# Kernel tuning notes

Hardware: AMD Instinct MI355X
Metric: run time of the kernel (lower is better)

The kernel has to match this reference:

```python
import jax, jax.numpy as jnp
import numpy as np

# Grid constants from init_kwargs: output_shape = [1, 10, 200, 176, 64]
D, H, W, C = 10, 200, 176, 64
N_VOX = 30000


def _conv_block(x, w, scale, bias, stride, pad):
    # x: [N,C,D,H,W]; w: [O,I,kd,kh,kw]; ZeroPad3d then valid Conv3d,
    # then fused (inference) BatchNorm3d + ReLU.
    x = jnp.pad(x, ((0, 0), (0, 0), (pad[0], pad[0]), (pad[1], pad[1]), (pad[2], pad[2])))
    x = jax.lax.conv_general_dilated(
        x, w, window_strides=stride, padding='VALID',
        dimension_numbers=('NCDHW', 'OIDHW', 'NCDHW'))
    s = scale[None, :, None, None, None]
    b = bias[None, :, None, None, None]
    return jax.nn.relu(x * s + b)


def setup_inputs() -> dict:
    key = jax.random.key(0)
    kf, kd, kh, kw, k1, k2, k3, ks = jax.random.split(key, 8)
    voxel_features = jax.random.normal(kf, (N_VOX, C), dtype=jnp.float32)
    # coors columns: (batch_idx, d, h, w) each in range
    b_idx = jnp.zeros((N_VOX,), dtype=jnp.int32)  # batch_size = 1
    d_idx = jax.random.randint(kd, (N_VOX,), 0, D, dtype=jnp.int32)
    h_idx = jax.random.randint(kh, (N_VOX,), 0, H, dtype=jnp.int32)
    w_idx = jax.random.randint(kw, (N_VOX,), 0, W, dtype=jnp.int32)
    coors = jnp.stack([b_idx, d_idx, h_idx, w_idx], axis=1)
    fan = 1.0 / np.sqrt(C * 27)
    W1 = jax.random.normal(k1, (64, C, 3, 3, 3), dtype=jnp.float32) * fan
    W2 = jax.random.normal(k2, (64, 64, 3, 3, 3), dtype=jnp.float32) * fan
    W3 = jax.random.normal(k3, (64, 64, 3, 3, 3), dtype=jnp.float32) * fan
    ks1, ks2, ks3 = jax.random.split(ks, 3)
    scale1 = jax.random.uniform(ks1, (64,), dtype=jnp.float32, minval=0.5, maxval=1.5)
    scale2 = jax.random.uniform(ks2, (64,), dtype=jnp.float32, minval=0.5, maxval=1.5)
    scale3 = jax.random.uniform(ks3, (64,), dtype=jnp.float32, minval=0.5, maxval=1.5)
    bias1 = jax.random.normal(jax.random.fold_in(ks1, 1), (64,), dtype=jnp.float32) * 0.1
    bias2 = jax.random.normal(jax.random.fold_in(ks2, 1), (64,), dtype=jnp.float32) * 0.1
    bias3 = jax.random.normal(jax.random.fold_in(ks3, 1), (64,), dtype=jnp.float32) * 0.1
    return {
        'voxel_features': voxel_features, 'coors': coors, 'batch_size': 1,
        'W1': W1, 'scale1': scale1, 'bias1': bias1,
        'W2': W2, 'scale2': scale2, 'bias2': bias2,
        'W3': W3, 'scale3': scale3, 'bias3': bias3,
    }


def reference(voxel_features, coors, batch_size,
              W1, scale1, bias1, W2, scale2, bias2, W3, scale3, bias3):
    # scatter_nd: sparse voxel features -> dense [B, D, H, W, C]
    dense = jnp.zeros((batch_size, D, H, W, C), dtype=voxel_features.dtype)
    dense = dense.at[coors[:, 0], coors[:, 1], coors[:, 2], coors[:, 3]].set(voxel_features)
    x = dense.transpose(0, 4, 1, 2, 3)  # [B, C, D, H, W]
    # middle_conv: Pad(1)+Conv3d s=(2,1,1); Pad(0,1,1)+Conv3d s=1; Pad(1)+Conv3d s=(2,1,1)
    x = _conv_block(x, W1, scale1, bias1, (2, 1, 1), (1, 1, 1))   # D: 10 -> 5
    x = _conv_block(x, W2, scale2, bias2, (1, 1, 1), (0, 1, 1))   # D: 5 -> 3
    x = _conv_block(x, W3, scale3, bias3, (2, 1, 1), (1, 1, 1))   # D: 3 -> 2
    N, Cc, Dd, Hh, Ww = x.shape
    return x.reshape(N, Cc * Dd, Hh, Ww)  # [B, 128, H, W]
```

## Files before the change

kernel.cpp:

```cpp
#include <hip/hip_runtime.h>
#include <cstddef>

#define HH 200
#define WW 176
#define HP 202
#define WP 178
#define D_IN 10
#define D1 5
#define D2 3
#define D3 2
#define SLICE ((size_t)HP * WP * 64)

#define LA_BYTES 38912

typedef _Float16 h8 __attribute__((ext_vector_type(8)));
typedef float f4 __attribute__((ext_vector_type(4)));

__device__ __forceinline__ void gl_lds16(const void* g, void* l) {
    __builtin_amdgcn_global_load_lds(
        (const __attribute__((address_space(1))) void*)g,
        (__attribute__((address_space(3))) void*)l, 16, 0, 0);
}

__global__ __launch_bounds__(256) void prep_k(const float* __restrict__ W1,
                                              const float* __restrict__ W2,
                                              const float* __restrict__ W3,
                                              _Float16* __restrict__ wdst,
                                              _Float16* __restrict__ A2,
                                              _Float16* __restrict__ A3,
                                              const int* __restrict__ coors,
                                              int* __restrict__ winner, int nvox) {
    const int b = blockIdx.x;
    if (b < 8) {
        _Float16* base = (b < D1) ? (A2 + (size_t)b * SLICE) : (A3 + (size_t)(b - D1) * SLICE);
        const h8 z = {};
        for (int t = threadIdx.x; t < 6080; t += 256) {
            size_t off;
            if (t < 2848) {
                int r = t / 1424, c = t - r * 1424;
                off = (size_t)(r ? (HP - 1) : 0) * WP * 64 + (size_t)c * 8;
            } else {
                int u = t - 2848;
                int c = u / 1616, v = u - c * 1616;
                int hr = v >> 3, o = v & 7;
                off = ((size_t)hr * WP + (c ? (WP - 1) : 0)) * 64 + (size_t)o * 8;
            }
            *(h8*)(base + off) = z;
        }
    } else if (b < 8 + 1296) {
        int idx = (b - 8) * 256 + threadIdx.x;
        if (idx < 3 * 27 * 64 * 64) {
            int set = idx / 110592;
            int r = idx - set * 110592;
            const float* src = set == 0 ? W1 : (set == 1 ? W2 : W3);
            int ci = r & 63;
            int co = (r >> 6) & 63;
            int tap = r >> 12;
            wdst[set * 110592 + tap * 4096 + (ci >> 3) * 512 + co * 8 + (ci & 7)] =
                (_Float16)src[(co * 64 + ci) * 27 + tap];
        }
    } else {
        int v = (b - 1304) * 256 + threadIdx.x;
        if (v < nvox) {
            int d = coors[v * 4 + 1], h = coors[v * 4 + 2], w = coors[v * 4 + 3];
            atomicMax(&winner[(d * HH + h) * WW + w], v + 1);
        }
    }
}

__global__ __launch_bounds__(256) void scatter_k(const float* __restrict__ feat,
                                                 const int* __restrict__ coors,
                                                 const int* __restrict__ winner,
                                                 _Float16* __restrict__ A, int nvox) {
    int v = blockIdx.x * 4 + (threadIdx.x >> 6);
    int ci = threadIdx.x & 63;
    if (v >= nvox) return;
    int d = coors[v * 4 + 1], h = coors[v * 4 + 2], w = coors[v * 4 + 3];
    if (winner[(d * HH + h) * WW + w] != v + 1) return;
    int P = w + 1;
    int swz = (((ci >> 3) ^ (P & 7)) << 3) | (ci & 7);
    A[(size_t)d * SLICE + ((size_t)(h + 1) * WP + P) * 64 + swz] = (_Float16)feat[v * 64 + ci];
}

template <int FINAL>
__global__ __launch_bounds__(256, 4) void conv_mfma_k(
    const _Float16* __restrict__ in, void* __restrict__ outp,
    const _Float16* __restrict__ wt,
    const float* __restrict__ scale, const float* __restrict__ bias,
    int inD, int strideD, int padD) {
    __shared__ char smem_raw[LA_BYTES];
    _Float16* la = (_Float16*)smem_raw;

    const int lane = threadIdx.x & 63;
    const int wave = threadIdx.x >> 6;
    const int l16 = lane & 15;
    const int quad = lane >> 4;
    const int h0 = blockIdx.y * 4;
    const int wb = blockIdx.x * 48;
    const int d = blockIdx.z;

    int kd_lo = padD - d * strideD; if (kd_lo < 0) kd_lo = 0;
    int kd_hi = inD - 1 - d * strideD + padD; if (kd_hi > 2) kd_hi = 2;

    f4 acc[3][4];
#pragma unroll
    for (int mt = 0; mt < 3; ++mt)
#pragma unroll
        for (int nt = 0; nt < 4; ++nt) acc[mt][nt] = (f4){0.f, 0.f, 0.f, 0.f};

    for (int kd = kd_lo; kd <= kd_hi; ++kd) {
        const int zd = d * strideD + kd - padD;
        const _Float16* __restrict__ aplane = in + (size_t)zd * SLICE;
        const _Float16* __restrict__ wkd = wt + (size_t)kd * 9 * 4096;

        __syncthreads();
        for (int j = wave; j < 38; j += 4) {
            int c = j * 64 + lane;
            if (c > 2399) c = 2399;
            int r = c / 400;
            int rem = c - r * 400;
            int px = rem >> 3, s = rem & 7;
            int g = wb + px; if (g > 177) g = 177;
            gl_lds16(aplane + ((size_t)(h0 + r) * WP + g) * 64 + s * 8,
                     smem_raw + j * 1024);
        }
        __syncthreads();

#pragma unroll
        for (int t = 0; t < 9; ++t) {
            const int kh = t / 3;
            const int kw = t - 3 * kh;

            h8 b[2][4];
#pragma unroll
            for (int ch = 0; ch < 2; ++ch)
#pragma unroll
                for (int nt = 0; nt < 4; ++nt)
                    b[ch][nt] = *(const h8*)(wkd + t * 4096 +
                                             ((ch * 4 + quad) << 9) +
                                             ((nt * 16 + l16) << 3));

#pragma unroll
            for (int ch = 0; ch < 2; ++ch) {
                const int q = ch * 4 + quad;
#pragma unroll
                for (int mt = 0; mt < 3; ++mt) {
                    const int px = mt * 16 + l16 + kw;
                    h8 a = *(const h8*)(la + ((wave + kh) * 50 + px) * 64 +
                                        ((q ^ (px & 7)) << 3));
#pragma unroll
                    for (int nt = 0; nt < 4; ++nt)
                        acc[mt][nt] = __builtin_amdgcn_mfma_f32_16x16x32_f16(
                            a, b[ch][nt], acc[mt][nt], 0, 0, 0);
                }
            }
        }
    }

    const int h = h0 + wave;
#pragma unroll
    for (int nt = 0; nt < 4; ++nt) {
        const int co = nt * 16 + l16;
        const float s = scale[co];
        const float bb = bias[co];
#pragma unroll
        for (int mt = 0; mt < 3; ++mt) {
            const int w0 = wb + mt * 16 + quad * 4;
            if (w0 < WW) {
                if (FINAL) {
                    f4 v;
#pragma unroll
                    for (int r = 0; r < 4; ++r) {
                        float x = acc[mt][nt][r] * s + bb;
                        v[r] = x > 0.f ? x : 0.f;
                    }
                    *(f4*)((float*)outp + (((size_t)(co * 2 + d)) * HH + h) * WW + w0) = v;
                } else {
#pragma unroll
                    for (int r = 0; r < 4; ++r) {
                        float x = acc[mt][nt][r] * s + bb;
                        x = x > 0.f ? x : 0.f;
                        const int P = w0 + r + 1;
                        const int swz = (((co >> 3) ^ (P & 7)) << 3) | (co & 7);
                        ((_Float16*)outp)[(size_t)d * SLICE +
                            ((size_t)(h + 1) * WP + P) * 64 + swz] = (_Float16)x;
                    }
                }
            }
        }
    }
}

extern "C" void kernel_launch(void* const* d_in, const int* in_sizes, int n_in,
                              void* d_out, int out_size, void* d_ws, size_t ws_size,
                              hipStream_t stream) {
    const float* feat   = (const float*)d_in[0];
    const int*   coors  = (const int*)d_in[1];
    const float* W1     = (const float*)d_in[3];
    const float* scale1 = (const float*)d_in[4];
    const float* bias1  = (const float*)d_in[5];
    const float* W2     = (const float*)d_in[6];
    const float* scale2 = (const float*)d_in[7];
    const float* bias2  = (const float*)d_in[8];
    const float* W3     = (const float*)d_in[9];
    const float* scale3 = (const float*)d_in[10];
    const float* bias3  = (const float*)d_in[11];
    const int nvox = in_sizes[0] / 64;

    const size_t nA1 = (size_t)D_IN * SLICE;
    const size_t nWin = (size_t)D_IN * HH * WW;
    const size_t nA2 = (size_t)D1 * SLICE;
    const size_t nA3 = (size_t)D2 * SLICE;
    const size_t nWT = (size_t)27 * 64 * 64;

    _Float16* A1 = (_Float16*)d_ws;
    int* win = (int*)(A1 + nA1);
    _Float16* A2 = (_Float16*)(win + nWin);
    _Float16* A3 = A2 + nA2;
    _Float16* wt1 = A3 + nA3;
    _Float16* wt2 = wt1 + nWT;
    _Float16* wt3 = wt2 + nWT;

    hipMemsetAsync(d_ws, 0, nA1 * sizeof(_Float16) + nWin * sizeof(int), stream);

    const int win_blk = (nvox + 255) / 256;
    prep_k<<<8 + 1296 + win_blk, 256, 0, stream>>>(W1, W2, W3, wt1, A2, A3,
                                                   coors, win, nvox);
    scatter_k<<<(nvox + 3) / 4, 256, 0, stream>>>(feat, coors, win, A1, nvox);

    dim3 blk(256);
    conv_mfma_k<0><<<dim3(4, 50, D1), blk, 0, stream>>>(A1, A2, wt1, scale1, bias1, D_IN, 2, 1);
    conv_mfma_k<0><<<dim3(4, 50, D2), blk, 0, stream>>>(A2, A3, wt2, scale2, bias2, D1, 1, 0);
    conv_mfma_k<1><<<dim3(4, 50, D3), blk, 0, stream>>>(A3, (float*)d_out, wt3, scale3, bias3, D2, 2, 1);
}
```

Measured before the change: 192.9 us.

## Compute two output rows per wave and prefetch next weight tap into registers

Each block now covers 8 output rows instead of 4, so each wave computes two rows and reuses every loaded weight fragment across twice as many MFMAs. The LDS input tile grows to 10 halo rows, which cuts the redundant halo reloads. The weights for the next kernel tap are double-buffered in registers so their global loads overlap the current tap's MFMAs. In exchange the grid halves, fewer blocks fit per CU (launch bound drops to 2), and register use and LDS per block rise, which lowers occupancy.

```diff
diff --git a/kernel.cpp b/kernel.cpp
--- a/kernel.cpp
+++ b/kernel.cpp
@@ -11,7 +11,7 @@
 #define D3 2
 #define SLICE ((size_t)HP * WP * 64)
 
-#define LA_BYTES 38912
+#define LA_BYTES 64512
 
 typedef _Float16 h8 __attribute__((ext_vector_type(8)));
 typedef float f4 __attribute__((ext_vector_type(4)));
@@ -83,7 +83,7 @@
 }
 
 template <int FINAL>
-__global__ __launch_bounds__(256, 4) void conv_mfma_k(
+__global__ __launch_bounds__(256, 2) void conv_mfma_k(
     const _Float16* __restrict__ in, void* __restrict__ outp,
     const _Float16* __restrict__ wt,
     const float* __restrict__ scale, const float* __restrict__ bias,
@@ -95,18 +95,20 @@
     const int wave = threadIdx.x >> 6;
     const int l16 = lane & 15;
     const int quad = lane >> 4;
-    const int h0 = blockIdx.y * 4;
+    const int h0 = blockIdx.y * 8;
     const int wb = blockIdx.x * 48;
     const int d = blockIdx.z;
 
     int kd_lo = padD - d * strideD; if (kd_lo < 0) kd_lo = 0;
     int kd_hi = inD - 1 - d * strideD + padD; if (kd_hi > 2) kd_hi = 2;
 
-    f4 acc[3][4];
-#pragma unroll
-    for (int mt = 0; mt < 3; ++mt)
-#pragma unroll
-        for (int nt = 0; nt < 4; ++nt) acc[mt][nt] = (f4){0.f, 0.f, 0.f, 0.f};
+    f4 acc[2][3][4];
+#pragma unroll
+    for (int rr = 0; rr < 2; ++rr)
+#pragma unroll
+        for (int mc = 0; mc < 3; ++mc)
+#pragma unroll
+            for (int nt = 0; nt < 4; ++nt) acc[rr][mc][nt] = (f4){0.f, 0.f, 0.f, 0.f};
 
     for (int kd = kd_lo; kd <= kd_hi; ++kd) {
         const int zd = d * strideD + kd - padD;
@@ -114,9 +116,9 @@
         const _Float16* __restrict__ wkd = wt + (size_t)kd * 9 * 4096;
 
         __syncthreads();
-        for (int j = wave; j < 38; j += 4) {
+        for (int j = wave; j < 63; j += 4) {
             int c = j * 64 + lane;
-            if (c > 2399) c = 2399;
+            if (c > 3999) c = 3999;
             int r = c / 400;
             int rem = c - r * 400;
             int px = rem >> 3, s = rem & 7;
@@ -124,6 +126,13 @@
             gl_lds16(aplane + ((size_t)(h0 + r) * WP + g) * 64 + s * 8,
                      smem_raw + j * 1024);
         }
+        h8 bc[2][4], bn[2][4];
+#pragma unroll
+        for (int ch = 0; ch < 2; ++ch)
+#pragma unroll
+            for (int nt = 0; nt < 4; ++nt)
+                bc[ch][nt] = *(const h8*)(wkd + ((ch * 4 + quad) << 9) +
+                                          ((nt * 16 + l16) << 3));
         __syncthreads();
 
 #pragma unroll
@@ -131,59 +140,75 @@
             const int kh = t / 3;
             const int kw = t - 3 * kh;
 
-            h8 b[2][4];
-#pragma unroll
-            for (int ch = 0; ch < 2; ++ch)
-#pragma unroll
-                for (int nt = 0; nt < 4; ++nt)
-                    b[ch][nt] = *(const h8*)(wkd + t * 4096 +
-                                             ((ch * 4 + quad) << 9) +
-                                             ((nt * 16 + l16) << 3));
+            if (t < 8) {
+#pragma unroll
+                for (int ch = 0; ch < 2; ++ch)
+#pragma unroll
+                    for (int nt = 0; nt < 4; ++nt)
+                        bn[ch][nt] = *(const h8*)(wkd + (t + 1) * 4096 +
+                                                  ((ch * 4 + quad) << 9) +
+                                                  ((nt * 16 + l16) << 3));
+            }
 
 #pragma unroll
             for (int ch = 0; ch < 2; ++ch) {
                 const int q = ch * 4 + quad;
 #pragma unroll
-                for (int mt = 0; mt < 3; ++mt) {
-                    const int px = mt * 16 + l16 + kw;
-                    h8 a = *(const h8*)(la + ((wave + kh) * 50 + px) * 64 +
-                                        ((q ^ (px & 7)) << 3));
+                for (int rr = 0; rr < 2; ++rr) {
+                    const int row = wave * 2 + rr + kh;
+#pragma unroll
+                    for (int mc = 0; mc < 3; ++mc) {
+                        const int px = mc * 16 + l16 + kw;
+                        h8 a = *(const h8*)(la + ((size_t)row * 50 + px) * 64 +
+                                            ((q ^ (px & 7)) << 3));
+#pragma unroll
+                        for (int nt = 0; nt < 4; ++nt)
+                            acc[rr][mc][nt] = __builtin_amdgcn_mfma_f32_16x16x32_f16(
+                                a, bc[ch][nt], acc[rr][mc][nt], 0, 0, 0);
+                    }
+                }
+            }
+
+            if (t < 8) {
+#pragma unroll
+                for (int ch = 0; ch < 2; ++ch)
 #pragma unroll
                     for (int nt = 0; nt < 4; ++nt)
-                        acc[mt][nt] = __builtin_amdgcn_mfma_f32_16x16x32_f16(
-                            a, b[ch][nt], acc[mt][nt], 0, 0, 0);
-                }
+                        bc[ch][nt] = bn[ch][nt];
             }
         }
     }
 
-    const int h = h0 + wave;
 #pragma unroll
     for (int nt = 0; nt < 4; ++nt) {
         const int co = nt * 16 + l16;
         const float s = scale[co];
         const float bb = bias[co];
 #pragma unroll
-        for (int mt = 0; mt < 3; ++mt) {
-            const int w0 = wb + mt * 16 + quad * 4;
-            if (w0 < WW) {
-                if (FINAL) {
-                    f4 v;
-#pragma unroll
-                    for (int r = 0; r < 4; ++r) {
-                        float x = acc[mt][nt][r] * s + bb;
-                        v[r] = x > 0.f ? x : 0.f;
-                    }
-                    *(f4*)((float*)outp + (((size_t)(co * 2 + d)) * HH + h) * WW + w0) = v;
-                } else {
-#pragma unroll
-                    for (int r = 0; r < 4; ++r) {
-                        float x = acc[mt][nt][r] * s + bb;
-                        x = x > 0.f ? x : 0.f;
-                        const int P = w0 + r + 1;
-                        const int swz = (((co >> 3) ^ (P & 7)) << 3) | (co & 7);
-                        ((_Float16*)outp)[(size_t)d * SLICE +
-                            ((size_t)(h + 1) * WP + P) * 64 + swz] = (_Float16)x;
+        for (int rr = 0; rr < 2; ++rr) {
+            const int h = h0 + wave * 2 + rr;
+#pragma unroll
+            for (int mc = 0; mc < 3; ++mc) {
+                const int w0 = wb + mc * 16 + quad * 4;
+                if (w0 < WW) {
+                    if (FINAL) {
+                        f4 v;
+#pragma unroll
+                        for (int r = 0; r < 4; ++r) {
+                            float x = acc[rr][mc][nt][r] * s + bb;
+                            v[r] = x > 0.f ? x : 0.f;
+                        }
+                        *(f4*)((float*)outp + (((size_t)(co * 2 + d)) * HH + h) * WW + w0) = v;
+                    } else {
+#pragma unroll
+                        for (int r = 0; r < 4; ++r) {
+                            float x = acc[rr][mc][nt][r] * s + bb;
+                            x = x > 0.f ? x : 0.f;
+                            const int P = w0 + r + 1;
+                            const int swz = (((co >> 3) ^ (P & 7)) << 3) | (co & 7);
+                            ((_Float16*)outp)[(size_t)d * SLICE +
+                                ((size_t)(h + 1) * WP + P) * 64 + swz] = (_Float16)x;
+                        }
                     }
                 }
             }
@@ -229,7 +254,7 @@
     scatter_k<<<(nvox + 3) / 4, 256, 0, stream>>>(feat, coors, win, A1, nvox);
 
     dim3 blk(256);
-    conv_mfma_k<0><<<dim3(4, 50, D1), blk, 0, stream>>>(A1, A2, wt1, scale1, bias1, D_IN, 2, 1);
-    conv_mfma_k<0><<<dim3(4, 50, D2), blk, 0, stream>>>(A2, A3, wt2, scale2, bias2, D1, 1, 0);
-    conv_mfma_k<1><<<dim3(4, 50, D3), blk, 0, stream>>>(A3, (float*)d_out, wt3, scale3, bias3, D2, 2, 1);
-}
+    conv_mfma_k<0><<<dim3(4, 25, D1), blk, 0, stream>>>(A1, A2, wt1, scale1, bias1, D_IN, 2, 1);
+    conv_mfma_k<0><<<dim3(4, 25, D2), blk, 0, stream>>>(A2, A3, wt2, scale2, bias2, D1, 1, 0);
+    conv_mfma_k<1><<<dim3(4, 25, D3), blk, 0, stream>>>(A3, (float*)d_out, wt3, scale3, bias3, D2, 2, 1);
+}
```

New measurement: 230.4 us. 19.4% more time.

## Software-pipeline weight fragment loads and stage fp16 epilogue through LDS

Applied to the files above, without the earlier changes.

Splits the 9-tap loop into 18 half-channel steps and prefetches the next step's weight fragments into registers while the current MFMAs run. This is meant to hide global/L2 latency of the B operand. For the intermediate (non-final) layers, results are first written to a padded per-wave LDS tile and then stored as 16-byte swizzled vectors instead of scattered 2-byte stores. This reduces global store transactions at the cost of an extra barrier, LDS traffic and more live registers.

```diff
diff --git a/kernel.cpp b/kernel.cpp
--- a/kernel.cpp
+++ b/kernel.cpp
@@ -124,50 +124,54 @@
             gl_lds16(aplane + ((size_t)(h0 + r) * WP + g) * 64 + s * 8,
                      smem_raw + j * 1024);
         }
+        h8 bc[4], bn[4];
+#pragma unroll
+        for (int nt = 0; nt < 4; ++nt)
+            bc[nt] = *(const h8*)(wkd + (quad << 9) + ((nt * 16 + l16) << 3));
         __syncthreads();
 
 #pragma unroll
-        for (int t = 0; t < 9; ++t) {
+        for (int p = 0; p < 18; ++p) {
+            const int t = p >> 1;
+            const int ch = p & 1;
             const int kh = t / 3;
             const int kw = t - 3 * kh;
-
-            h8 b[2][4];
-#pragma unroll
-            for (int ch = 0; ch < 2; ++ch)
+            const int q = ch * 4 + quad;
+
+            const int pn = (p < 17) ? p + 1 : 17;
+            const int tn = pn >> 1, chn = pn & 1;
+#pragma unroll
+            for (int nt = 0; nt < 4; ++nt)
+                bn[nt] = *(const h8*)(wkd + tn * 4096 + ((chn * 4 + quad) << 9) +
+                                      ((nt * 16 + l16) << 3));
+
+#pragma unroll
+            for (int mt = 0; mt < 3; ++mt) {
+                const int px = mt * 16 + l16 + kw;
+                h8 a = *(const h8*)(la + ((size_t)(wave + kh) * 50 + px) * 64 +
+                                    ((q ^ (px & 7)) << 3));
 #pragma unroll
                 for (int nt = 0; nt < 4; ++nt)
-                    b[ch][nt] = *(const h8*)(wkd + t * 4096 +
-                                             ((ch * 4 + quad) << 9) +
-                                             ((nt * 16 + l16) << 3));
-
-#pragma unroll
-            for (int ch = 0; ch < 2; ++ch) {
-                const int q = ch * 4 + quad;
-#pragma unroll
-                for (int mt = 0; mt < 3; ++mt) {
-                    const int px = mt * 16 + l16 + kw;
-                    h8 a = *(const h8*)(la + ((wave + kh) * 50 + px) * 64 +
-                                        ((q ^ (px & 7)) << 3));
-#pragma unroll
-                    for (int nt = 0; nt < 4; ++nt)
-                        acc[mt][nt] = __builtin_amdgcn_mfma_f32_16x16x32_f16(
-                            a, b[ch][nt], acc[mt][nt], 0, 0, 0);
-                }
-            }
+                    acc[mt][nt] = __builtin_amdgcn_mfma_f32_16x16x32_f16(
+                        a, bc[nt], acc[mt][nt], 0, 0, 0);
+            }
+
+#pragma unroll
+            for (int nt = 0; nt < 4; ++nt) bc[nt] = bn[nt];
         }
     }
 
     const int h = h0 + wave;
-#pragma unroll
-    for (int nt = 0; nt < 4; ++nt) {
-        const int co = nt * 16 + l16;
-        const float s = scale[co];
-        const float bb = bias[co];
-#pragma unroll
-        for (int mt = 0; mt < 3; ++mt) {
-            const int w0 = wb + mt * 16 + quad * 4;
-            if (w0 < WW) {
-                if (FINAL) {
+    if (FINAL) {
+#pragma unroll
+        for (int nt = 0; nt < 4; ++nt) {
+            const int co = nt * 16 + l16;
+            const float s = scale[co];
+            const float bb = bias[co];
+#pragma unroll
+            for (int mt = 0; mt < 3; ++mt) {
+                const int w0 = wb + mt * 16 + quad * 4;
+                if (w0 < WW) {
                     f4 v;
 #pragma unroll
                     for (int r = 0; r < 4; ++r) {
@@ -175,17 +179,37 @@
                         v[r] = x > 0.f ? x : 0.f;
                     }
                     *(f4*)((float*)outp + (((size_t)(co * 2 + d)) * HH + h) * WW + w0) = v;
-                } else {
-#pragma unroll
-                    for (int r = 0; r < 4; ++r) {
-                        float x = acc[mt][nt][r] * s + bb;
-                        x = x > 0.f ? x : 0.f;
-                        const int P = w0 + r + 1;
-                        const int swz = (((co >> 3) ^ (P & 7)) << 3) | (co & 7);
-                        ((_Float16*)outp)[(size_t)d * SLICE +
-                            ((size_t)(h + 1) * WP + P) * 64 + swz] = (_Float16)x;
-                    }
                 }
+            }
+        }
+    } else {
+        __syncthreads();
+        _Float16* ep = (_Float16*)smem_raw + (size_t)wave * (48 * 72);
+#pragma unroll
+        for (int nt = 0; nt < 4; ++nt) {
+            const int co = nt * 16 + l16;
+            const float s = scale[co];
+            const float bb = bias[co];
+#pragma unroll
+            for (int mt = 0; mt < 3; ++mt) {
+#pragma unroll
+                for (int r = 0; r < 4; ++r) {
+                    float x = acc[mt][nt][r] * s + bb;
+                    x = x > 0.f ? x : 0.f;
+                    ep[(mt * 16 + quad * 4 + r) * 72 + co] = (_Float16)x;
+                }
+            }
+        }
+        const int lim = (WW - wb) * 8;
+#pragma unroll
+        for (int cv = 0; cv < 6; ++cv) {
+            if (cv * 64 < lim) {
+                const int c2 = cv * 64 + lane;
+                const int pxl = c2 >> 3, s = c2 & 7;
+                h8 v = *(const h8*)(ep + pxl * 72 + s * 8);
+                const int P = wb + pxl + 1;
+                *(h8*)((_Float16*)outp + (size_t)d * SLICE +
+                       ((size_t)(h + 1) * WP + P) * 64 + ((s ^ (P & 7)) << 3)) = v;
             }
         }
     }
```

New measurement: 191.3 us. No clear change (-0.8%).
